# Optimization experiments

Hardware: AMD Instinct MI355X
Metric: run time of the kernel (lower is better)

## Reference

```python
import jax, jax.numpy as jnp
import numpy as np

B, S, D, H = 4, 2048, 1024, 16
HD = D // H


def setup_inputs() -> dict:
    key = jax.random.key(0)
    ks = jax.random.split(key, 5)
    scale = 1.0 / np.sqrt(D)
    return {
        "x": jax.random.normal(ks[0], (B, S, D), dtype=jnp.float32),
        "W_q": jax.random.normal(ks[1], (D, D), dtype=jnp.float32) * scale,
        "W_k": jax.random.normal(ks[2], (D, D), dtype=jnp.float32) * scale,
        "W_v": jax.random.normal(ks[3], (D, D), dtype=jnp.float32) * scale,
        "W_o": jax.random.normal(ks[4], (D, D), dtype=jnp.float32) * scale,
    }


def reference(x, W_q, W_k, W_v, W_o):
    # Linear with weight [out, in]: y = x @ W^T
    def proj(W):
        return jnp.einsum('bsd,ed->bshf', x, W.reshape(H, HD, D).transpose(0, 1, 2).reshape(D, D)) if False else (x @ W.T).reshape(B, S, H, HD).transpose(0, 2, 1, 3)

    q = proj(W_q)  # [B, H, S, HD]
    k = proj(W_k)
    v = proj(W_v)

    scores = jnp.einsum('bhqd,bhkd->bhqk', q, k) / jnp.sqrt(jnp.float32(HD))
    causal = jnp.triu(jnp.ones((S, S), dtype=bool), k=1)  # True above diagonal -> masked
    scores = jnp.where(causal, -jnp.inf, scores)
    probs = jax.nn.softmax(scores, axis=-1)
    out = jnp.einsum('bhqk,bhkd->bhqd', probs, v)  # [B, H, S, HD]
    out = out.transpose(0, 2, 1, 3).reshape(B, S, D)
    return out @ W_o.T
```

## Files before the change

### kernel.cpp

```cpp
#include <hip/hip_runtime.h>
#include <cstdint>
#include <cstddef>

typedef unsigned short u16;
typedef __attribute__((ext_vector_type(8))) short short8;
typedef __attribute__((ext_vector_type(4))) short short4v;
typedef __attribute__((ext_vector_type(8))) unsigned short ushort8v;
typedef __attribute__((ext_vector_type(4))) unsigned short ushort4v;
typedef __attribute__((ext_vector_type(4))) unsigned int uint4v;
typedef __attribute__((ext_vector_type(4))) float f32x4;

#define QSCALE 0.18033688011112042f
#define THR_L2 11.5417f


__device__ __forceinline__ u16 f2bf(float f) {
  unsigned int u = __builtin_bit_cast(unsigned int, f);
  u += 0x7FFFu + ((u >> 16) & 1u);
  return (u16)(u >> 16);
}

__device__ __forceinline__ void async16(const void* g, void* l) {
  __builtin_amdgcn_global_load_lds(
      (const __attribute__((address_space(1))) unsigned int*)g,
      (__attribute__((address_space(3))) unsigned int*)l, 16, 0, 0);
}

__device__ __forceinline__ float fmax3(float a, float b, float c) {
  float r;
  asm("v_max3_f32 %0, %1, %2, %3" : "=v"(r) : "v"(a), "v"(b), "v"(c));
  return r;
}

__device__ __forceinline__ unsigned int cvtpk(float lo, float hi) {
  unsigned int r;
  asm("v_cvt_pk_bf16_f32 %0, %1, %2" : "=v"(r) : "v"(lo), "v"(hi));
  return r;
}


__global__ void cvt_all(const float* __restrict__ x, const float* __restrict__ Wq,
                        const float* __restrict__ Wk, const float* __restrict__ Wv,
                        const float* __restrict__ Wo, u16* __restrict__ out) {
  const int bid = blockIdx.x;
  const float* src;
  int i;
  size_t doff;
  if (bid < 8192) {
    i = bid * 1024 + threadIdx.x * 4;
    src = x;
    doff = (size_t)i;
  } else {
    const int k = bid - 8192;
    const int wsel = k >> 10;
    i = (k & 1023) * 1024 + threadIdx.x * 4;
    src = (wsel == 0) ? Wq : (wsel == 1) ? Wk : (wsel == 2) ? Wv : Wo;
    doff = 8388608 + (size_t)wsel * 1048576 + i;
  }
  float4 v = *(const float4*)(src + i);
  ushort4v o;
  o[0] = f2bf(v.x); o[1] = f2bf(v.y); o[2] = f2bf(v.z); o[3] = f2bf(v.w);
  *(ushort4v*)(out + doff) = o;
}


template<int MODE>
__global__ __launch_bounds__(512, 1) void gemm_qb(
    const u16* __restrict__ A, const u16* __restrict__ Bw,
    void* __restrict__ Cout, int M, int N, int K)
{
  const int t = threadIdx.x;
  const int lane = t & 63, w = t >> 6;
  const int li = lane & 15, g = lane >> 4;
  const int wm = w >> 1, wn = w & 1;

  const int nx = gridDim.x;
  const int hwid = blockIdx.y * nx + blockIdx.x;
  const int cpx = (nx * gridDim.y) >> 3;
  const int lid = (hwid & 7) * cpx + (hwid >> 3);
  const int brow = (lid / nx) * 256, bcol = (lid % nx) * 128;

  __shared__ u16 As[4][256 * 32];
  __shared__ u16 Bs[4][128 * 32];

  f32x4 acc[4][4];
#pragma unroll
  for (int i = 0; i < 4; ++i)
#pragma unroll
    for (int j = 0; j < 4; ++j) acc[i][j] = f32x4{0.f, 0.f, 0.f, 0.f};

  auto STAGE = [&](int T) {
    const int b = T & 3;
    const int k0 = T * 32;
#pragma unroll
    for (int L = 0; L < 2; ++L) {
      const int f2 = t + 512 * L;
      const int row = f2 >> 2;
      const int cb = ((f2 & 3) * 16) ^ (((row >> 1) & 3) << 4);
      async16(A + (size_t)(brow + row) * K + k0 + (cb >> 1), &As[b][f2 * 8]);
    }
    const int rowb = t >> 2;
    const int cbb = ((t & 3) * 16) ^ (((rowb >> 1) & 3) << 4);
    async16(Bw + (size_t)(bcol + rowb) * K + k0 + (cbb >> 1), &Bs[b][t * 8]);
  };

  STAGE(0); STAGE(1); STAGE(2);

  const int NT = K >> 5;
  const int ksw = (g * 8) ^ (((li >> 1) & 3) << 3);

#pragma unroll 1
  for (int T = 0; T < NT; ++T) {
    if (T < NT - 2)      asm volatile("s_waitcnt vmcnt(6)" ::: "memory");
    else if (T == NT - 2) asm volatile("s_waitcnt vmcnt(3)" ::: "memory");
    else                  asm volatile("s_waitcnt vmcnt(0)" ::: "memory");
    asm volatile("s_barrier" ::: "memory");
    const int b = T & 3;
    short8 af[4], bfr[4];
#pragma unroll
    for (int mt = 0; mt < 4; ++mt)
      af[mt] = *(const short8*)&As[b][(wm * 64 + mt * 16 + li) * 32 + ksw];
#pragma unroll
    for (int nt = 0; nt < 4; ++nt)
      bfr[nt] = *(const short8*)&Bs[b][(wn * 64 + nt * 16 + li) * 32 + ksw];

    if (T + 3 < NT) STAGE(T + 3);

    __builtin_amdgcn_s_setprio(1);
#pragma unroll
    for (int mt = 0; mt < 4; ++mt)
#pragma unroll
      for (int nt = 0; nt < 4; ++nt)
        acc[mt][nt] = __builtin_amdgcn_mfma_f32_16x16x32_bf16(af[mt], bfr[nt], acc[mt][nt], 0, 0, 0);
    __builtin_amdgcn_s_setprio(0);
  }

#pragma unroll
  for (int mt = 0; mt < 4; ++mt)
#pragma unroll
    for (int nt = 0; nt < 4; ++nt) {
      const int col = bcol + wn * 64 + nt * 16 + li;
#pragma unroll
      for (int r = 0; r < 4; ++r) {
        const int row = brow + wm * 64 + mt * 16 + g * 4 + r;
        float v = acc[mt][nt][r];
        if (MODE == 0) {
          const int which = col >> 10;
          const int c2 = col & 1023;
          if (which == 0) v *= QSCALE;
          const int bb = row >> 11, s = row & 2047;
          const int h = c2 >> 6, hd = c2 & 63;
          ((u16*)Cout)[(size_t)which * 8388608 +
                       (((size_t)(bb * 16 + h) * 2048) + s) * 64 + hd] = f2bf(v);
        } else {
          ((float*)Cout)[(size_t)row * N + col] = v;
        }
      }
    }
}


__global__ __launch_bounds__(256) void transpose_hd_s(
    const u16* __restrict__ V, u16* __restrict__ VT)
{
  const int sb = blockIdx.x;
  const int bh = blockIdx.y;
  __shared__ u16 tile[64 * 72];
  const int t = threadIdx.x;
  const int r = t >> 3;
  const int c8 = (t & 7) * 8;
  const size_t base = (size_t)bh * 2048 * 64;
#pragma unroll
  for (int half = 0; half < 2; ++half) {
    const int row = r + 32 * half;
    ushort8v v = *(const ushort8v*)(V + base + (size_t)(sb * 64 + row) * 64 + c8);
    *(ushort8v*)&tile[row * 72 + c8] = v;
  }
  __syncthreads();
#pragma unroll
  for (int half = 0; half < 2; ++half) {
    const int hd = r + 32 * half;
    ushort8v o;
#pragma unroll
    for (int j = 0; j < 8; ++j) {
      const int pos = c8 + j;
      const int kv = (pos & 32) + (((pos >> 2) & 1) << 4) + (((pos >> 3) & 3) << 2) + (pos & 3);
      o[j] = tile[kv * 72 + hd];
    }
    *(ushort8v*)(VT + base + (size_t)hd * 2048 + sb * 64 + c8) = o;
  }
}


__global__ __launch_bounds__(256, 2) void flash_attn9(
    const u16* __restrict__ Qp, const u16* __restrict__ Kp,
    const u16* __restrict__ VTp, u16* __restrict__ Oattn)
{
  const int hwid = blockIdx.x;
  const int lid = (hwid & 7) * 64 + (hwid >> 3);
  const int pr = lid & 7, bh = lid >> 3;

  const int t = threadIdx.x;
  const int lane = t & 63, w = t >> 6;
  const int li = lane & 15, g = lane >> 4;

  __shared__ u16 Kl[3][64 * 64];
  __shared__ u16 Vl[3][64 * 64];

  const size_t bh_off = (size_t)bh * (2048 * 64);
  const int tile0 = pr, tile1 = 15 - pr;
  const int njb0 = 2 * tile0 + 2;

  short8 qf0[2][2], qf1[2][2];
#pragma unroll
  for (int qs = 0; qs < 2; ++qs) {
    const u16* qp0 = Qp + bh_off + (size_t)(tile0 * 128 + qs * 64 + w * 16 + li) * 64 + g * 8;
    qf0[qs][0] = *(const short8*)qp0;
    qf0[qs][1] = *(const short8*)(qp0 + 32);
    const u16* qp1 = Qp + bh_off + (size_t)(tile1 * 128 + qs * 64 + w * 16 + li) * 64 + g * 8;
    qf1[qs][0] = *(const short8*)qp1;
    qf1[qs][1] = *(const short8*)(qp1 + 32);
  }
  short8 qc[2][2];
#pragma unroll
  for (int qs = 0; qs < 2; ++qs) { qc[qs][0] = qf0[qs][0]; qc[qs][1] = qf0[qs][1]; }

  int qbase = tile0 * 128;

  short8 onesf;
#pragma unroll
  for (int j = 0; j < 8; ++j) onesf[j] = (short)0x3F80;

  f32x4 o_acc[2][4];
  f32x4 osum[2];
#pragma unroll
  for (int qs = 0; qs < 2; ++qs) {
    osum[qs] = f32x4{0.f, 0.f, 0.f, 0.f};
#pragma unroll
    for (int i = 0; i < 4; ++i) o_acc[qs][i] = f32x4{0.f, 0.f, 0.f, 0.f};
  }
  float m_i[2] = {-1e30f, -1e30f};

  const int b = bh >> 4, h = bh & 15;
  const int ksw = (li & 7) << 3;

  auto STAGE = [&](int i, int s) {
    const int jb = (i < njb0) ? i : (i - njb0);
#pragma unroll
    for (int L = 0; L < 2; ++L) {
      const int f = t + 256 * L;
      const int kbyte = (f * 16) ^ (((f >> 3) & 7) << 4);
      async16(Kp + bh_off + (size_t)jb * 4096 + (kbyte >> 1),
              &Kl[s][(w * 64 + 256 * L) * 8]);
      const int vrow = f >> 3;
      const int vb = ((f & 7) * 16) ^ ((vrow & 7) << 4);
      async16(VTp + bh_off + (size_t)vrow * 2048 + jb * 64 + (vb >> 1),
              &Vl[s][(w * 64 + 256 * L) * 8]);
    }
  };

  auto WRITEO = [&]() {
#pragma unroll
    for (int qs = 0; qs < 2; ++qs) {
      const float inv_l = 1.f / osum[qs][0];
      const int qrow = qbase + qs * 64 + w * 16 + li;
      u16* op = Oattn + ((size_t)(b * 2048 + qrow)) * 1024 + h * 64;
#pragma unroll
      for (int dt = 0; dt < 4; ++dt) {
        ushort4v st;
#pragma unroll
        for (int r = 0; r < 4; ++r) st[r] = f2bf(o_acc[qs][dt][r] * inv_l);
        *(ushort4v*)(op + dt * 16 + g * 4) = st;
      }
    }
  };

  STAGE(0, 0);
  STAGE(1, 1);
  asm volatile("s_waitcnt vmcnt(4)" ::: "memory");
  __builtin_amdgcn_s_barrier();

#pragma unroll 1
  for (int i = 0; i < 34; ++i) {
    const int s = i % 3;
    if (i + 2 < 34) STAGE(i + 2, (i + 2) % 3);

    const int jb = (i < njb0) ? i : (i - njb0);
    const u16* __restrict__ Ks = &Kl[s][0];
    const u16* __restrict__ Vs = &Vl[s][0];

    f32x4 s_acc[2][4];
#pragma unroll
    for (int qs = 0; qs < 2; ++qs)
#pragma unroll
      for (int jt = 0; jt < 4; ++jt) s_acc[qs][jt] = f32x4{0.f, 0.f, 0.f, 0.f};
    __builtin_amdgcn_s_setprio(1);
#pragma unroll
    for (int kc = 0; kc < 2; ++kc)
#pragma unroll
      for (int jt = 0; jt < 4; ++jt) {
        short8 kf = *(const short8*)&Ks[(jt * 16 + li) * 64 + ((kc * 32 + g * 8) ^ ksw)];
        s_acc[0][jt] = __builtin_amdgcn_mfma_f32_16x16x32_bf16(kf, qc[0][kc], s_acc[0][jt], 0, 0, 0);
        s_acc[1][jt] = __builtin_amdgcn_mfma_f32_16x16x32_bf16(kf, qc[1][kc], s_acc[1][jt], 0, 0, 0);
      }
    __builtin_amdgcn_s_setprio(0);

    float mx[2];
    bool need = false;
#pragma unroll
    for (int qs = 0; qs < 2; ++qs) {
      if (jb * 64 + 63 > qbase + qs * 64 + w * 16) {
        const int tq = qbase + qs * 64 + w * 16 + li - jb * 64;
#pragma unroll
        for (int jt = 0; jt < 4; ++jt)
#pragma unroll
          for (int r = 0; r < 4; ++r)
            if (jt * 16 + g * 4 + r > tq) s_acc[qs][jt][r] = -1e30f;
      }
      float t0 = fmax3(s_acc[qs][0][0], s_acc[qs][0][1], s_acc[qs][0][2]);
      float t1 = fmax3(s_acc[qs][0][3], s_acc[qs][1][0], s_acc[qs][1][1]);
      float t2 = fmax3(s_acc[qs][1][2], s_acc[qs][1][3], s_acc[qs][2][0]);
      float t3 = fmax3(s_acc[qs][2][1], s_acc[qs][2][2], s_acc[qs][2][3]);
      float t4m = fmax3(s_acc[qs][3][0], s_acc[qs][3][1], s_acc[qs][3][2]);
      float m01 = fmax3(t0, t1, s_acc[qs][3][3]);
      float m23 = fmax3(t2, t3, t4m);
      float mm = fmaxf(m01, m23);
      mm = fmaxf(mm, __shfl_xor(mm, 16));
      mm = fmaxf(mm, __shfl_xor(mm, 32));
      mx[qs] = mm;
      need = need || (mm > m_i[qs] + THR_L2);
    }

    if (__any((int)need)) {
#pragma unroll
      for (int qs = 0; qs < 2; ++qs) {
        const float mn = fmaxf(m_i[qs], mx[qs]);
        const float corr = __builtin_amdgcn_exp2f(m_i[qs] - mn);
        osum[qs] *= corr;
#pragma unroll
        for (int dt = 0; dt < 4; ++dt) o_acc[qs][dt] *= corr;
        m_i[qs] = mn;
      }
    }

    short8 pf[2][2];
#pragma unroll
    for (int qs = 0; qs < 2; ++qs) {
      const float mi = m_i[qs];
#pragma unroll
      for (int jt = 0; jt < 4; ++jt)
#pragma unroll
        for (int r = 0; r < 4; ++r)
          s_acc[qs][jt][r] = __builtin_amdgcn_exp2f(s_acc[qs][jt][r] - mi);
#pragma unroll
      for (int kc = 0; kc < 2; ++kc) {
        uint4v u;
        u[0] = cvtpk(s_acc[qs][2 * kc][0], s_acc[qs][2 * kc][1]);
        u[1] = cvtpk(s_acc[qs][2 * kc][2], s_acc[qs][2 * kc][3]);
        u[2] = cvtpk(s_acc[qs][2 * kc + 1][0], s_acc[qs][2 * kc + 1][1]);
        u[3] = cvtpk(s_acc[qs][2 * kc + 1][2], s_acc[qs][2 * kc + 1][3]);
        pf[qs][kc] = __builtin_bit_cast(short8, u);
      }
    }

    __builtin_amdgcn_s_setprio(1);
#pragma unroll
    for (int kc = 0; kc < 2; ++kc) {
      osum[0] = __builtin_amdgcn_mfma_f32_16x16x32_bf16(onesf, pf[0][kc], osum[0], 0, 0, 0);
      osum[1] = __builtin_amdgcn_mfma_f32_16x16x32_bf16(onesf, pf[1][kc], osum[1], 0, 0, 0);
#pragma unroll
      for (int dt = 0; dt < 4; ++dt) {
        short8 vf = *(const short8*)&Vs[(dt * 16 + li) * 64 + ((kc * 32 + g * 8) ^ ksw)];
        o_acc[0][dt] = __builtin_amdgcn_mfma_f32_16x16x32_bf16(vf, pf[0][kc], o_acc[0][dt], 0, 0, 0);
        o_acc[1][dt] = __builtin_amdgcn_mfma_f32_16x16x32_bf16(vf, pf[1][kc], o_acc[1][dt], 0, 0, 0);
      }
    }
    __builtin_amdgcn_s_setprio(0);

    asm volatile("s_waitcnt lgkmcnt(0)" ::: "memory");
    if (i < 32) { asm volatile("s_waitcnt vmcnt(4)" ::: "memory"); }
    else        { asm volatile("s_waitcnt vmcnt(0)" ::: "memory"); }
    __builtin_amdgcn_s_barrier();

    if (i == njb0 - 1) {
      WRITEO();
      qbase = tile1 * 128;
#pragma unroll
      for (int qs = 0; qs < 2; ++qs) {
        qc[qs][0] = qf1[qs][0]; qc[qs][1] = qf1[qs][1];
        m_i[qs] = -1e30f;
        osum[qs] = f32x4{0.f, 0.f, 0.f, 0.f};
#pragma unroll
        for (int dt = 0; dt < 4; ++dt) o_acc[qs][dt] = f32x4{0.f, 0.f, 0.f, 0.f};
      }
    }
  }

  WRITEO();
}


extern "C" void kernel_launch(void* const* d_in, const int* in_sizes, int n_in,
                              void* d_out, int out_size, void* d_ws, size_t ws_size,
                              hipStream_t stream) {
  const float* x  = (const float*)d_in[0];
  const float* Wq = (const float*)d_in[1];
  const float* Wk = (const float*)d_in[2];
  const float* Wv = (const float*)d_in[3];
  const float* Wo = (const float*)d_in[4];

  const size_t NX = 8388608;
  const size_t NW = 1048576;

  u16* xb  = (u16*)d_ws;
  u16* wqb = xb + NX;
  u16* wob = wqb + 3 * NW;
  u16* Qb  = wob + NW;
  u16* Kb  = Qb + NX;
  u16* Vb  = Kb + NX;
  u16* VTb = Vb + NX;
  u16* attnb = Vb;

  cvt_all<<<12288, 256, 0, stream>>>(x, Wq, Wk, Wv, Wo, xb);

  gemm_qb<0><<<dim3(24, 32), 512, 0, stream>>>(xb, wqb, Qb, 8192, 3072, 1024);

  transpose_hd_s<<<dim3(32, 64), 256, 0, stream>>>(Vb, VTb);
  flash_attn9<<<512, 256, 0, stream>>>(Qb, Kb, VTb, attnb);

  gemm_qb<1><<<dim3(8, 32), 512, 0, stream>>>(attnb, wob, d_out, 8192, 1024, 1024);
}
```

Measured before the change: 167.5 us.

## Fuse V transpose into QKV GEMM epilogue and shrink GEMM pipeline to 3 stages

The QKV projection GEMM now writes V straight into the permuted transposed layout that flash attention expects, with 4-element vector stores, so the separate transpose kernel and its extra read/write pass over V are removed. The GEMM's LDS ring buffer goes from 4 to 3 stages (prefetch distance 2), and launch bounds now ask for 4 blocks per CU, which cuts shared memory per block and may allow more resident blocks. The shorter prefetch distance could expose more load latency, and the transposed V stores are strided across hd rows.

```diff
diff --git a/kernel.cpp b/kernel.cpp
--- a/kernel.cpp
+++ b/kernel.cpp
@@ -65,7 +65,7 @@
 
 
 template<int MODE>
-__global__ __launch_bounds__(512, 1) void gemm_qb(
+__global__ __launch_bounds__(512, 4) void gemm_tb(
     const u16* __restrict__ A, const u16* __restrict__ Bw,
     void* __restrict__ Cout, int M, int N, int K)
 {
@@ -80,8 +80,8 @@
   const int lid = (hwid & 7) * cpx + (hwid >> 3);
   const int brow = (lid / nx) * 256, bcol = (lid % nx) * 128;
 
-  __shared__ u16 As[4][256 * 32];
-  __shared__ u16 Bs[4][128 * 32];
+  __shared__ u16 As[3][256 * 32];
+  __shared__ u16 Bs[3][128 * 32];
 
   f32x4 acc[4][4];
 #pragma unroll
@@ -90,7 +90,7 @@
     for (int j = 0; j < 4; ++j) acc[i][j] = f32x4{0.f, 0.f, 0.f, 0.f};
 
   auto STAGE = [&](int T) {
-    const int b = T & 3;
+    const int b = T % 3;
     const int k0 = T * 32;
 #pragma unroll
     for (int L = 0; L < 2; ++L) {
@@ -104,18 +104,17 @@
     async16(Bw + (size_t)(bcol + rowb) * K + k0 + (cbb >> 1), &Bs[b][t * 8]);
   };
 
-  STAGE(0); STAGE(1); STAGE(2);
+  STAGE(0); STAGE(1);
 
   const int NT = K >> 5;
   const int ksw = (g * 8) ^ (((li >> 1) & 3) << 3);
 
 #pragma unroll 1
   for (int T = 0; T < NT; ++T) {
-    if (T < NT - 2)      asm volatile("s_waitcnt vmcnt(6)" ::: "memory");
-    else if (T == NT - 2) asm volatile("s_waitcnt vmcnt(3)" ::: "memory");
-    else                  asm volatile("s_waitcnt vmcnt(0)" ::: "memory");
+    if (T < NT - 1) asm volatile("s_waitcnt vmcnt(3)" ::: "memory");
+    else            asm volatile("s_waitcnt vmcnt(0)" ::: "memory");
     asm volatile("s_barrier" ::: "memory");
-    const int b = T & 3;
+    const int b = T % 3;
     short8 af[4], bfr[4];
 #pragma unroll
     for (int mt = 0; mt < 4; ++mt)
@@ -124,7 +123,7 @@
     for (int nt = 0; nt < 4; ++nt)
       bfr[nt] = *(const short8*)&Bs[b][(wn * 64 + nt * 16 + li) * 32 + ksw];
 
-    if (T + 3 < NT) STAGE(T + 3);
+    if (T + 2 < NT) STAGE(T + 2);
 
     __builtin_amdgcn_s_setprio(1);
 #pragma unroll
@@ -140,55 +139,36 @@
 #pragma unroll
     for (int nt = 0; nt < 4; ++nt) {
       const int col = bcol + wn * 64 + nt * 16 + li;
-#pragma unroll
-      for (int r = 0; r < 4; ++r) {
-        const int row = brow + wm * 64 + mt * 16 + g * 4 + r;
-        float v = acc[mt][nt][r];
-        if (MODE == 0) {
-          const int which = col >> 10;
-          const int c2 = col & 1023;
-          if (which == 0) v *= QSCALE;
-          const int bb = row >> 11, s = row & 2047;
-          const int h = c2 >> 6, hd = c2 & 63;
-          ((u16*)Cout)[(size_t)which * 8388608 +
-                       (((size_t)(bb * 16 + h) * 2048) + s) * 64 + hd] = f2bf(v);
+      const int row0 = brow + wm * 64 + mt * 16 + g * 4;
+      if (MODE == 1) {
+#pragma unroll
+        for (int r = 0; r < 4; ++r)
+          ((float*)Cout)[(size_t)(row0 + r) * N + col] = acc[mt][nt][r];
+      } else {
+        const int which = col >> 10;
+        const int c2 = col & 1023;
+        const int h = c2 >> 6, hd = c2 & 63;
+        const int bb = row0 >> 11, s0 = row0 & 2047;
+        if (which == 2) {
+          const int kv = s0 & 63;
+          const int pos = (kv & 0x23) | ((kv & 0x10) >> 2) | ((kv & 0x0C) << 1);
+          ushort4v st;
+#pragma unroll
+          for (int r = 0; r < 4; ++r) st[r] = f2bf(acc[mt][nt][r]);
+          *(ushort4v*)((u16*)Cout + (size_t)3 * 8388608 +
+                       (size_t)(bb * 16 + h) * 131072 + (size_t)hd * 2048 +
+                       (s0 >> 6) * 64 + pos) = st;
         } else {
-          ((float*)Cout)[(size_t)row * N + col] = v;
+#pragma unroll
+          for (int r = 0; r < 4; ++r) {
+            float v = acc[mt][nt][r];
+            if (which == 0) v *= QSCALE;
+            ((u16*)Cout)[(size_t)which * 8388608 +
+                         (((size_t)(bb * 16 + h) * 2048) + s0 + r) * 64 + hd] = f2bf(v);
+          }
         }
       }
     }
-}
-
-
-__global__ __launch_bounds__(256) void transpose_hd_s(
-    const u16* __restrict__ V, u16* __restrict__ VT)
-{
-  const int sb = blockIdx.x;
-  const int bh = blockIdx.y;
-  __shared__ u16 tile[64 * 72];
-  const int t = threadIdx.x;
-  const int r = t >> 3;
-  const int c8 = (t & 7) * 8;
-  const size_t base = (size_t)bh * 2048 * 64;
-#pragma unroll
-  for (int half = 0; half < 2; ++half) {
-    const int row = r + 32 * half;
-    ushort8v v = *(const ushort8v*)(V + base + (size_t)(sb * 64 + row) * 64 + c8);
-    *(ushort8v*)&tile[row * 72 + c8] = v;
-  }
-  __syncthreads();
-#pragma unroll
-  for (int half = 0; half < 2; ++half) {
-    const int hd = r + 32 * half;
-    ushort8v o;
-#pragma unroll
-    for (int j = 0; j < 8; ++j) {
-      const int pos = c8 + j;
-      const int kv = (pos & 32) + (((pos >> 2) & 1) << 4) + (((pos >> 3) & 3) << 2) + (pos & 3);
-      o[j] = tile[kv * 72 + hd];
-    }
-    *(ushort8v*)(VT + base + (size_t)hd * 2048 + sb * 64 + c8) = o;
-  }
 }
 
 
@@ -417,16 +397,14 @@
   u16* wob = wqb + 3 * NW;
   u16* Qb  = wob + NW;
   u16* Kb  = Qb + NX;
-  u16* Vb  = Kb + NX;
-  u16* VTb = Vb + NX;
-  u16* attnb = Vb;
+  u16* VTb = Qb + 3 * NX;
+  u16* attnb = Qb + 2 * NX;
 
   cvt_all<<<12288, 256, 0, stream>>>(x, Wq, Wk, Wv, Wo, xb);
 
-  gemm_qb<0><<<dim3(24, 32), 512, 0, stream>>>(xb, wqb, Qb, 8192, 3072, 1024);
-
-  transpose_hd_s<<<dim3(32, 64), 256, 0, stream>>>(Vb, VTb);
+  gemm_tb<0><<<dim3(24, 32), 512, 0, stream>>>(xb, wqb, Qb, 8192, 3072, 1024);
+
   flash_attn9<<<512, 256, 0, stream>>>(Qb, Kb, VTb, attnb);
 
-  gemm_qb<1><<<dim3(8, 32), 512, 0, stream>>>(attnb, wob, d_out, 8192, 1024, 1024);
-}
+  gemm_tb<1><<<dim3(8, 32), 512, 0, stream>>>(attnb, wob, d_out, 8192, 1024, 1024);
+}
```

Result: faster. 157.1 us (-6.2%).
